# Kernel tuning notes

Hardware: AMD Instinct MI355X
Metric: run time of the kernel (lower is better)

## Reference

```python
import jax, jax.numpy as jnp
import numpy as np

B, N2, N3, D = 16, 1024, 2048, 128


def setup_inputs() -> dict:
    key = jax.random.key(0)
    k1, k2 = jax.random.split(key)
    desc2d = jax.random.normal(k1, (B * N2, D), dtype=jnp.float32)
    desc3d = jax.random.normal(k2, (B * N3, D), dtype=jnp.float32)
    # uniform, sorted batch ids (equal-size segments -> jit-friendly ragged layout)
    idx2d = jnp.repeat(jnp.arange(B, dtype=jnp.int64), N2)
    idx3d = jnp.repeat(jnp.arange(B, dtype=jnp.int64), N3)
    return {"desc2d": desc2d, "idx2d": idx2d, "desc3d": desc3d, "idx3d": idx3d}


def reference(desc2d, idx2d, desc3d, idx3d):
    # number of batches from sorted batch ids (static, computed on host)
    nb = int(np.asarray(idx2d)[-1]) + 1
    n2 = desc2d.shape[0] // nb
    n3 = desc3d.shape[0] // nb
    d2 = desc2d.reshape(nb, n2, -1)  # [B, n2, D]
    d3 = desc3d.reshape(nb, n3, -1)  # [B, n3, D]
    d2 = d2 / jnp.linalg.norm(d2, axis=-1, keepdims=True)
    d3 = d3 / jnp.linalg.norm(d3, axis=-1, keepdims=True)
    sim = jnp.einsum('bid,bjd->bij', d3, d2)  # cosine similarity [B, n3, n2]
    # zero-pad one extra row and column per batch (dustbin), as in the original
    return jnp.pad(sim, ((0, 0), (0, 1), (0, 1)))
```

## Files before the change

kernel.cpp:

```cpp
#include <hip/hip_runtime.h>
#include <hip/hip_bf16.h>

#define NB   16
#define N2   1024
#define N3   2048
#define DD   128
#define OROWS (N3 + 1)
#define OCOLS (N2 + 1)

typedef __attribute__((ext_vector_type(8))) __bf16 bf16x8;
typedef __attribute__((ext_vector_type(4))) float  f32x4;

static __device__ __forceinline__ unsigned pack_bf16x2(float a, float b) {
    unsigned ua = __float_as_uint(a);
    ua = (ua + 0x7FFF + ((ua >> 16) & 1)) >> 16;
    unsigned ub = __float_as_uint(b);
    ub = (ub + 0x7FFF + ((ub >> 16) & 1)) & 0xFFFF0000u;
    return ua | ub;
}

__global__ void normalize_d2(const float* __restrict__ d2,
                             unsigned short* __restrict__ ws) {
    const int row = blockIdx.x * 8 + (threadIdx.x >> 5);
    const int l   = threadIdx.x & 31;
    const float4 v = *reinterpret_cast<const float4*>(d2 + (size_t)row * DD + l * 4);
    float ss = v.x * v.x + v.y * v.y + v.z * v.z + v.w * v.w;
    #pragma unroll
    for (int off = 16; off; off >>= 1) ss += __shfl_xor(ss, off);
    const float s = rsqrtf(ss);
    uint2 w;
    w.x = pack_bf16x2(v.x * s, v.y * s);
    w.y = pack_bf16x2(v.z * s, v.w * s);
    *reinterpret_cast<uint2*>(ws + (size_t)row * DD + l * 4) = w;
}

__global__ __launch_bounds__(256, 4)
void gemm_kernel(const float* __restrict__ d3,
                 const unsigned short* __restrict__ d2n,
                 float* __restrict__ out) {
    __shared__ __align__(16) char smem[40960];

    const int hw  = blockIdx.x;
    const int blk = (hw & 7) * 64 + (hw >> 3);
    const int b   = blk >> 5;
    const int ti  = blk & 31;
    const int t   = threadIdx.x;

    const float* gA = d3 + (size_t)(b * N3 + ti * 64) * DD;
    const char*  gB = (const char*)d2n + ((size_t)(b * N2) << 8);

    char* const aLds = smem + 24576;

    auto stage = [&](int c) {
        const char* src = gB + (size_t)c * 8192;
        char* dst = smem + 8192 * (c % 3);
        #pragma unroll
        for (int it = 0; it < 2; ++it) {
            int o    = it * 4096 + t * 16;
            int row  = o >> 8;
            int scol = (o & 255) ^ ((row & 7) << 4);
            __builtin_amdgcn_global_load_lds(
                (const __attribute__((address_space(1))) void*)(src + row * 256 + scol),
                (__attribute__((address_space(3))) void*)(dst + o), 16, 0, 0);
        }
    };

    const int arow  = t >> 2;
    const int apart = t & 3;
    float4 av[8];
    #pragma unroll
    for (int i = 0; i < 8; ++i)
        av[i] = *reinterpret_cast<const float4*>(gA + (size_t)arow * DD + apart * 32 + i * 4);
    stage(0);

    {
        float ss = 0.f;
        #pragma unroll
        for (int i = 0; i < 8; ++i)
            ss += av[i].x * av[i].x + av[i].y * av[i].y + av[i].z * av[i].z + av[i].w * av[i].w;
        ss += __shfl_xor(ss, 1);
        ss += __shfl_xor(ss, 2);
        const float s = rsqrtf(ss);
        const int aswz = (arow & 7) << 4;
        #pragma unroll
        for (int j = 0; j < 4; ++j) {
            uint4 w;
            w.x = pack_bf16x2(av[2 * j].x * s,     av[2 * j].y * s);
            w.y = pack_bf16x2(av[2 * j].z * s,     av[2 * j].w * s);
            w.z = pack_bf16x2(av[2 * j + 1].x * s, av[2 * j + 1].y * s);
            w.w = pack_bf16x2(av[2 * j + 1].z * s, av[2 * j + 1].w * s);
            int colb = apart * 64 + j * 16;
            *reinterpret_cast<uint4*>(aLds + arow * 256 + (colb ^ aswz)) = w;
        }
    }
    asm volatile("s_waitcnt vmcnt(0) lgkmcnt(0)" ::: "memory");
    __builtin_amdgcn_s_barrier();
    __builtin_amdgcn_sched_barrier(0);

    const int wid = t >> 6;
    const int l   = t & 63;
    const int wm  = wid * 16;
    const int lr  = l & 15;
    const int kq  = l >> 4;
    const int sw  = (lr & 7) << 4;

    bf16x8 af[4];
    #pragma unroll
    for (int ks = 0; ks < 4; ++ks) {
        const int kb = ks * 64 + kq * 16;
        af[ks] = *reinterpret_cast<const bf16x8*>(aLds + (wm + lr) * 256 + (kb ^ sw));
    }

    float* obase = out + (size_t)b * OROWS * OCOLS + (size_t)(ti * 64) * OCOLS;

    for (int nj = 0; nj < 32; ++nj) {
        const char* bbuf = smem + 8192 * (nj % 3);

        f32x4 acc[2] = {};
        #pragma unroll
        for (int ks = 0; ks < 4; ++ks) {
            const int kb = ks * 64 + kq * 16;
            #pragma unroll
            for (int ni = 0; ni < 2; ++ni) {
                bf16x8 bfr = *reinterpret_cast<const bf16x8*>(
                    bbuf + (ni * 16 + lr) * 256 + (kb ^ sw));
                acc[ni] = __builtin_amdgcn_mfma_f32_16x16x32_bf16(
                    af[ks], bfr, acc[ni], 0, 0, 0);
            }
        }

        if (nj == 0) { stage(1); stage(2); }
        else if (nj + 2 < 32) stage(nj + 2);

        #pragma unroll
        for (int i = 0; i < 4; ++i) {
            int r = wm + kq * 4 + i;
            #pragma unroll
            for (int ni = 0; ni < 2; ++ni) {
                int c = nj * 32 + ni * 16 + lr;
                obase[(size_t)r * OCOLS + c] = acc[ni][i];
            }
        }

        if (nj < 30) {
            asm volatile("s_waitcnt vmcnt(10)" ::: "memory");
            __builtin_amdgcn_s_barrier();
            __builtin_amdgcn_sched_barrier(0);
        } else if (nj == 30) {
            asm volatile("s_waitcnt vmcnt(8)" ::: "memory");
            __builtin_amdgcn_s_barrier();
            __builtin_amdgcn_sched_barrier(0);
        }
    }

    if (t < 64)
        obase[(size_t)t * OCOLS + N2] = 0.0f;
    if (ti == 31) {
        float* last = out + (size_t)b * OROWS * OCOLS + (size_t)N3 * OCOLS;
        for (int c = t; c < OCOLS; c += 256) last[c] = 0.0f;
    }
}

extern "C" void kernel_launch(void* const* d_in, const int* in_sizes, int n_in,
                              void* d_out, int out_size, void* d_ws, size_t ws_size,
                              hipStream_t stream) {
    (void)in_sizes; (void)n_in; (void)out_size; (void)ws_size;
    const float* desc2d = (const float*)d_in[0];
    const float* desc3d = (const float*)d_in[2];

    unsigned short* d2n = (unsigned short*)d_ws;
    float* out = (float*)d_out;

    normalize_d2<<<(NB * N2) / 8, 256, 0, stream>>>(desc2d, d2n);
    gemm_kernel<<<NB * (N3 / 64), 256, 0, stream>>>(desc3d, d2n, out);
}
```

Measured before the change: 39.35 us.

## Batch output stores over four N-chunks and rotate chunk start per block

Accumulates four 32-column chunks in registers and writes them together as 128-column bursts, instead of storing after every chunk. Each block also starts its column sweep at a different offset, spreading concurrent writes and d2 reads across memory channels. The vmcnt waits are retuned for fewer outstanding stores per barrier. This raises accumulator register pressure and groups the stores into bursts.

Result: slower. 41.44 us (+5.3%).

```diff
diff --git a/kernel.cpp b/kernel.cpp
--- a/kernel.cpp
+++ b/kernel.cpp
@@ -45,15 +45,17 @@
     const int b   = blk >> 5;
     const int ti  = blk & 31;
     const int t   = threadIdx.x;
+    const int cs  = (hw >> 3) & 3;
 
     const float* gA = d3 + (size_t)(b * N3 + ti * 64) * DD;
     const char*  gB = (const char*)d2n + ((size_t)(b * N2) << 8);
 
     char* const aLds = smem + 24576;
 
-    auto stage = [&](int c) {
+    auto stage = [&](int nj) {
+        const int  c   = (cs * 4 + nj) & 31;
         const char* src = gB + (size_t)c * 8192;
-        char* dst = smem + 8192 * (c % 3);
+        char* dst = smem + 8192 * (nj % 3);
         #pragma unroll
         for (int it = 0; it < 2; ++it) {
             int o    = it * 4096 + t * 16;
@@ -113,43 +115,52 @@
 
     float* obase = out + (size_t)b * OROWS * OCOLS + (size_t)(ti * 64) * OCOLS;
 
-    for (int nj = 0; nj < 32; ++nj) {
-        const char* bbuf = smem + 8192 * (nj % 3);
-
-        f32x4 acc[2] = {};
-        #pragma unroll
-        for (int ks = 0; ks < 4; ++ks) {
-            const int kb = ks * 64 + kq * 16;
-            #pragma unroll
-            for (int ni = 0; ni < 2; ++ni) {
-                bf16x8 bfr = *reinterpret_cast<const bf16x8*>(
-                    bbuf + (ni * 16 + lr) * 256 + (kb ^ sw));
-                acc[ni] = __builtin_amdgcn_mfma_f32_16x16x32_bf16(
-                    af[ks], bfr, acc[ni], 0, 0, 0);
-            }
-        }
-
-        if (nj == 0) { stage(1); stage(2); }
-        else if (nj + 2 < 32) stage(nj + 2);
+    for (int mc = 0; mc < 8; ++mc) {
+        f32x4 macc[4][2] = {};
 
         #pragma unroll
-        for (int i = 0; i < 4; ++i) {
-            int r = wm + kq * 4 + i;
+        for (int mi = 0; mi < 4; ++mi) {
+            const int nj = mc * 4 + mi;
+            const char* bbuf = smem + 8192 * (nj % 3);
+
             #pragma unroll
-            for (int ni = 0; ni < 2; ++ni) {
-                int c = nj * 32 + ni * 16 + lr;
-                obase[(size_t)r * OCOLS + c] = acc[ni][i];
+            for (int ks = 0; ks < 4; ++ks) {
+                const int kb = ks * 64 + kq * 16;
+                #pragma unroll
+                for (int ni = 0; ni < 2; ++ni) {
+                    bf16x8 bfr = *reinterpret_cast<const bf16x8*>(
+                        bbuf + (ni * 16 + lr) * 256 + (kb ^ sw));
+                    macc[mi][ni] = __builtin_amdgcn_mfma_f32_16x16x32_bf16(
+                        af[ks], bfr, macc[mi][ni], 0, 0, 0);
+                }
             }
-        }
 
-        if (nj < 30) {
-            asm volatile("s_waitcnt vmcnt(10)" ::: "memory");
-            __builtin_amdgcn_s_barrier();
-            __builtin_amdgcn_sched_barrier(0);
-        } else if (nj == 30) {
-            asm volatile("s_waitcnt vmcnt(8)" ::: "memory");
-            __builtin_amdgcn_s_barrier();
-            __builtin_amdgcn_sched_barrier(0);
+            if (mi == 3) {
+                const int cb = ((cs + mc) & 7) * 128;
+                #pragma unroll
+                for (int i = 0; i < 4; ++i) {
+                    const size_t rofs = (size_t)(wm + kq * 4 + i) * OCOLS;
+                    #pragma unroll
+                    for (int mmi = 0; mmi < 4; ++mmi)
+                        #pragma unroll
+                        for (int ni = 0; ni < 2; ++ni)
+                            obase[rofs + cb + mmi * 32 + ni * 16 + lr] =
+                                macc[mmi][ni][i];
+                }
+            }
+
+            if (nj == 0)            { stage(1); stage(2); }
+            else if (nj + 2 < 32)   stage(nj + 2);
+
+            if (nj < 30) {
+                asm volatile("s_waitcnt vmcnt(2)" ::: "memory");
+                __builtin_amdgcn_s_barrier();
+                __builtin_amdgcn_sched_barrier(0);
+            } else if (nj == 30) {
+                asm volatile("s_waitcnt vmcnt(0)" ::: "memory");
+                __builtin_amdgcn_s_barrier();
+                __builtin_amdgcn_sched_barrier(0);
+            }
         }
     }
 
```
